# Kernel optimization log

Hardware: AMD Instinct MI355X
Metric: run time of the kernel (lower is better)

Reference implementation:

```python
import jax, jax.numpy as jnp
import numpy as np

DIM, FFN, GC, NSET, K = 48, 2, 2, 32, 3
HID = DIM * FFN          # 96 hidden features
G = HID // GC            # 48 groups in KBA
CG = HID // G            # 2 channels per group
INTERC = 24              # min(dim, 24)
B, H, W = 4, 128, 128


def _conv(x, w, b=None, groups=1, pad=0):
    out = jax.lax.conv_general_dilated(
        x, w, (1, 1), [(pad, pad), (pad, pad)],
        dimension_numbers=('NCHW', 'OIHW', 'NCHW'),
        feature_group_count=groups)
    if b is not None:
        out = out + b[None, :, None, None]
    return out


def _kba(x, att, k, g, bb, ww):
    # x: [B,c,H,W], att: [B,nset,H,W], bb: [1,nset,c], ww: [1,nset,c*c//g*k*k]
    Bz, c, Hh, Ww = x.shape
    KK = k * k
    cg = c // g
    P = Hh * Ww
    a = att.reshape(Bz, -1, P).transpose(0, 2, 1)                     # [B,P,nset]
    bias = jnp.einsum('bpn,nc->bpc', a, bb[0])                        # [B,P,c]
    attk = jnp.einsum('bpn,nm->bpm', a, ww[0]).reshape(Bz, P, g, cg, cg * KK)
    pd = k // 2
    xp = jnp.pad(x, ((0, 0), (0, 0), (pd, pd), (pd, pd)))
    # im2col patches, torch.unfold layout: channel-major, kernel row-major
    patches = jnp.stack([xp[:, :, i:i + Hh, j:j + Ww]
                         for i in range(k) for j in range(k)], axis=2)  # [B,c,KK,H,W]
    uf = patches.reshape(Bz, g, cg * KK, P).transpose(0, 3, 1, 2)       # [B,P,g,cg*KK]
    out = jnp.einsum('bpgom,bpgm->bpgo', attk, uf).reshape(Bz, P, c) + bias
    return out.transpose(0, 2, 1).reshape(Bz, c, Hh, Ww)


def setup_inputs() -> dict:
    key = jax.random.key(0)
    ks = jax.random.split(key, 20)
    s = 0.05
    inp = {
        'x': jax.random.normal(ks[0], (B, DIM, H, W), jnp.float32),
        'dw1_w': jax.random.normal(ks[1], (HID, DIM, 1, 1), jnp.float32) * s,
        'dw2_w': jax.random.normal(ks[2], (HID, 1, 3, 3), jnp.float32) * s,
        'proj_w': jax.random.normal(ks[3], (DIM, HID, 1, 1), jnp.float32) * s,
        'sca_w': jax.random.normal(ks[4], (HID, HID, 1, 1), jnp.float32) * s,
        'sca_b': jax.random.normal(ks[5], (HID,), jnp.float32) * s,
        'c1_w1': jax.random.normal(ks[6], (HID, DIM, 1, 1), jnp.float32) * s,
        'c1_w2': jax.random.normal(ks[7], (HID, 1, 3, 3), jnp.float32) * s,
        'kba_w': jax.random.normal(ks[8], (1, NSET, HID * CG * K * K), jnp.float32) * s,
        'kba_b': jax.random.normal(ks[9], (1, NSET, HID), jnp.float32) * s,
        'c2_w1': jax.random.normal(ks[10], (INTERC, DIM // INTERC, 3, 3), jnp.float32) * s,
        'c2_b1': jax.random.normal(ks[11], (INTERC,), jnp.float32) * s,
        'c2_w2': jax.random.normal(ks[12], (NSET, INTERC // 2, 1, 1), jnp.float32) * s,
        'c2_b2': jax.random.normal(ks[13], (NSET,), jnp.float32) * s,
        'c211_w': jax.random.normal(ks[14], (NSET, DIM, 1, 1), jnp.float32) * s,
        'c211_b': jax.random.normal(ks[15], (NSET,), jnp.float32) * s,
        'attgamma': jnp.full((1, NSET, 1, 1), 0.01, jnp.float32),
        'ga1': jnp.full((1, HID, 1, 1), 0.01, jnp.float32),
    }
    return inp


def reference(x, dw1_w, dw2_w, proj_w, sca_w, sca_b, c1_w1, c1_w2,
              kba_w, kba_b, c2_w1, c2_b1, c2_w2, c2_b2,
              c211_w, c211_b, attgamma, ga1):
    # dwconv branch: 1x1 -> depthwise 3x3
    x1 = _conv(_conv(x, dw1_w), dw2_w, groups=HID, pad=1)
    # attention map branch: grouped 3x3 -> SimpleGate -> 1x1, scaled + skip 1x1
    t = _conv(x, c2_w1, c2_b1, groups=INTERC, pad=1)
    t1, t2 = jnp.split(t, 2, axis=1)
    t = _conv(t1 * t2, c2_w2, c2_b2)
    att = t * attgamma + _conv(x, c211_w, c211_b)
    # conv1 branch feeding KBA
    uf = _conv(_conv(x, c1_w1), c1_w2, groups=HID, pad=1)
    x2 = _kba(uf, att, K, G, kba_b, kba_w) * ga1 + uf
    comb = jax.nn.gelu(x1, approximate=False) * x2
    pooled = jnp.mean(comb, axis=(2, 3), keepdims=True)
    comb = comb * _conv(pooled, sca_w, sca_b)
    return _conv(comb, proj_w)
```

## Files before the change

kernel.cpp:

```cpp
#include <hip/hip_runtime.h>
#include <math.h>

#define BB 4
#define HH 128
#define WW 128
#define HWP (HH*WW)
#define DIMC 48
#define HIDC 96
#define NSETC 32

#define XS_W 27
#define HS_W 102
#define US_W 102

typedef __attribute__((ext_vector_type(8))) short bf16x8;
typedef __attribute__((ext_vector_type(4))) float f32x4;
typedef __attribute__((ext_vector_type(2))) float f32x2;

static __device__ __forceinline__ unsigned short f2bf(float f) {
    union { float f; unsigned u; } v; v.f = f;
    unsigned r = (v.u + 0x7FFFu + ((v.u >> 16) & 1u)) >> 16;
    return (unsigned short)r;
}
static __device__ __forceinline__ unsigned rnd_bf(float f) {
    union { float f; unsigned u; } v; v.f = f;
    return v.u + 0x8000u;
}
static __device__ __forceinline__ unsigned pack2bf(float lo, float hi) {
    return __builtin_amdgcn_perm(rnd_bf(hi), rnd_bf(lo), 0x07060302u);
}
static __device__ __forceinline__ void st_bf_hi(unsigned short* p, float f) {
    *p = (unsigned short)(rnd_bf(f) >> 16);
}
static __device__ __forceinline__ float bf2f(unsigned short u) {
    union { unsigned u; float f; } v; v.u = ((unsigned)u) << 16;
    return v.f;
}
static __device__ __forceinline__ float bfpair_lo(unsigned pr) {
    union { unsigned u; float f; } v; v.u = pr << 16; return v.f;
}
static __device__ __forceinline__ float bfpair_hi(unsigned pr) {
    union { unsigned u; float f; } v; v.u = pr & 0xffff0000u; return v.f;
}
static __device__ __forceinline__ float gelu(float x) {
    return 0.5f * x * (1.0f + erff(x * 0.70710678118654752f));
}

__global__ __launch_bounds__(256) void k_prep(
    const float* __restrict__ x,
    const float* __restrict__ kbaw, const float* __restrict__ kbab,
    const float* __restrict__ dw1w, const float* __restrict__ c1w1,
    const float* __restrict__ ga1,  const float* __restrict__ c211w,
    const float* __restrict__ c2w2, const float* __restrict__ c2b2,
    const float* __restrict__ c211b, const float* __restrict__ attg,
    unsigned short* __restrict__ Bpk, unsigned short* __restrict__ Bpw,
    unsigned short* __restrict__ Aps, unsigned short* __restrict__ Ag,
    unsigned* __restrict__ x_p, float* __restrict__ pooled)
{
    __shared__ unsigned ts[256 * 26];
    int blk = blockIdx.x, tid = threadIdx.x;
    if (blk < 300) {
        int t = blk * 256 + tid;
        if (t < 61440) {
            int j = t & 7, lane = (t >> 3) & 63, tile = t >> 9;
            int chunk = tile / 10, nt = tile - chunk * 10;
            int m = lane & 15, qn = lane >> 4;
            int lc = 4 * nt + (m & 3);
            int o = lc / 20, tt = lc % 20;
            int c = (m >> 2) * 24 + 2 * chunk + o;
            int n = qn * 8 + j;
            float v = 0.f;
            if (tt < 18)       v = kbaw[n * 1728 + (c >> 1) * 36 + (c & 1) * 18 + tt] * ga1[c];
            else if (tt == 18) v = kbab[n * 96 + c] * ga1[c];
            Bpk[t] = f2bf(v);
        } else if (t < 73728) {
            int u = t - 61440;
            int s = u / 6144;
            int rem = u % 6144;
            int nt = rem >> 9;
            int lane = (rem >> 3) & 63, j = rem & 7;
            int k = s * 32 + ((lane >> 4) << 3) + j;
            int col = (nt << 4) + (lane & 15);
            float v = 0.f;
            if (k < 48) v = (col < 96) ? dw1w[col * 48 + k] : c1w1[(col - 96) * 48 + k];
            Bpw[u] = f2bf(v);
        } else if (t < 75776) {
            int u = t - 73728;
            int j = u & 7, lane = (u >> 3) & 63, tile = u >> 9;
            int kt = tile >> 1, nt2 = tile & 1;
            int m = lane & 15, qn = lane >> 4;
            int n = 8 * (m >> 2) + 4 * nt2 + (m & 3);
            int k = kt * 32 + qn * 8 + j;
            Aps[u] = f2bf(k < 48 ? c211w[n * 48 + k] : 0.f);
        } else if (t < 76800) {
            int u = t - 75776;
            int j = u & 7, lane = (u >> 3) & 63, nt2 = u >> 9;
            int m = lane & 15, qn = lane >> 4;
            int n = 8 * (m >> 2) + 4 * nt2 + (m & 3);
            int k = qn * 8 + j;
            float v = 0.f;
            if (k < 12)       v = c2w2[n * 12 + k] * attg[n];
            else if (k == 12) v = c2b2[n] * attg[n] + c211b[n];
            Ag[u] = f2bf(v);
        }
    } else {
        int xblk = blk - 300;
        if (xblk == 0) {
            for (int i = tid; i < BB * HIDC; i += 256) pooled[i] = 0.f;
        }
        int b = xblk >> 6;
        int p0 = (xblk & 63) << 8;
        const float* xb = x + (size_t)b * DIMC * HWP + p0;
        #pragma unroll
        for (int c2 = 0; c2 < 24; ++c2) {
            float lo = xb[(2 * c2) * HWP + tid];
            float hi = xb[(2 * c2 + 1) * HWP + tid];
            ts[tid * 26 + c2] = pack2bf(lo, hi);
        }
        __syncthreads();
        unsigned* dst = x_p + ((size_t)b * HWP + p0) * 24;
        for (int idx = tid; idx < 256 * 24; idx += 256) {
            int px = idx / 24, j2 = idx - px * 24;
            dst[px * 24 + j2] = ts[px * 26 + j2];
        }
    }
}

__global__ __launch_bounds__(512, 2) void k_mff(
    const unsigned* __restrict__ x_p,
    const uint4* __restrict__ BpkA, const uint4* __restrict__ Bpw,
    const uint4* __restrict__ Aps,  const uint4* __restrict__ Ag,
    const float* __restrict__ c1w2, const float* __restrict__ dw2w,
    const float* __restrict__ c2w1, const float* __restrict__ c2b1,
    unsigned* __restrict__ comb_bf, float* __restrict__ pooled)
{
    __shared__ __attribute__((aligned(16))) unsigned xs[144 * XS_W];
    __shared__ __attribute__((aligned(16))) unsigned short hsw[144 * HS_W];
    __shared__ unsigned short us2p[100 * US_W];
    __shared__ float wls[864 + 432 + 24];
    __shared__ float pooled_s[96];

    int lane = threadIdx.x, wy = threadIdx.y;
    int tid = wy * 64 + lane;
    int blk = blockIdx.x;
    int b = blk >> 8, ty = (blk >> 4) & 15, tx = blk & 15;
    int q = lane >> 4, i16 = lane & 15;
    int wh = wy >> 2;
    int wp = wy & 3;

    float* wats  = wls + 864;
    float* c2b1s = wls + 864 + 432;
    float* att_tf = (float*)hsw;

    if (tid < 96) pooled_s[tid] = 0.f;
    for (int idx = tid; idx < 864; idx += 512) {
        int t5 = idx / 96, c = idx - t5 * 96;
        wls[idx] = dw2w[c * 9 + t5];
    }
    for (int idx = tid; idx < 216; idx += 512) {
        int g = idx / 9, tap = idx - g * 9;
        wats[idx * 2]     = c2w1[g * 18 + tap];
        wats[idx * 2 + 1] = c2w1[g * 18 + 9 + tap];
    }
    if (tid < 24) c2b1s[tid] = c2b1[tid];
    for (int idx = tid; idx < 144 * 12; idx += 512) {
        int pos = idx / 12, jp = idx - pos * 12;
        int gy = ty * 8 - 2 + pos / 12, gx = tx * 8 - 2 + pos % 12;
        uint2 v = {0u, 0u};
        if (((unsigned)gy < (unsigned)HH) & ((unsigned)gx < (unsigned)WW))
            v = *(const uint2*)&x_p[((size_t)b * HWP + gy * WW + gx) * 24 + jp * 2];
        xs[pos * XS_W + jp * 2]     = v.x;
        xs[pos * XS_W + jp * 2 + 1] = v.y;
    }
    __syncthreads();

    int p_t = wp * 16 + i16;
    int pyT = p_t >> 3, pxT = p_t & 7;
    int gp = (ty * 8 + pyT) * WW + tx * 8 + pxT;
    uint4 z4 = {0u, 0u, 0u, 0u};

    #pragma unroll
    for (int ci = 0; ci < 3; ++ci) {
        int g = q * 6 + wh * 3 + ci;
        float acc = c2b1s[g];
        #pragma unroll
        for (int di = 0; di < 3; ++di)
          #pragma unroll
          for (int dj = 0; dj < 3; ++dj) {
              unsigned pr = xs[((pyT + 1 + di) * 12 + pxT + 1 + dj) * XS_W + g];
              f32x2 w2 = *(const f32x2*)&wats[(g * 9 + di * 3 + dj) * 2];
              acc += w2.x * bfpair_lo(pr) + w2.y * bfpair_hi(pr);
          }
        att_tf[p_t * XS_W + g] = acc;
    }
    __syncthreads();

    bf16x8 afrag;
    {
        int p26 = p_t * XS_W;
        unsigned tgd[4];
        #pragma unroll
        for (int i2 = 0; i2 < 4; ++i2) {
            int k0 = q * 8 + 2 * i2;
            int k1 = k0 + 1;
            float v0 = (k0 < 12) ? att_tf[p26 + k0] * att_tf[p26 + 12 + k0] : (k0 == 12 ? 1.f : 0.f);
            float v1 = (k1 < 12) ? att_tf[p26 + k1] * att_tf[p26 + 12 + k1] : (k1 == 12 ? 1.f : 0.f);
            tgd[i2] = pack2bf(v0, v1);
        }
        uint4 tgr = {tgd[0], tgd[1], tgd[2], tgd[3]};
        bf16x8 btg = __builtin_bit_cast(bf16x8, tgr);

        int cen = (pyT + 2) * 12 + (pxT + 2);
        int cb = cen * XS_W + q * 4;
        uint4 bx0r = {xs[cb], xs[cb + 1], xs[cb + 2], xs[cb + 3]};
        uint4 bx1r = z4;
        if (q < 2) {
            int cb2 = cen * XS_W + 16 + q * 4;
            bx1r.x = xs[cb2]; bx1r.y = xs[cb2 + 1]; bx1r.z = xs[cb2 + 2]; bx1r.w = xs[cb2 + 3];
        }
        bf16x8 bx0 = __builtin_bit_cast(bf16x8, bx0r);
        bf16x8 bx1 = __builtin_bit_cast(bf16x8, bx1r);

        float attv[8];
        #pragma unroll
        for (int nt2 = 0; nt2 < 2; ++nt2) {
            bf16x8 ag  = __builtin_bit_cast(bf16x8, Ag[nt2 * 64 + lane]);
            bf16x8 as0 = __builtin_bit_cast(bf16x8, Aps[nt2 * 64 + lane]);
            bf16x8 as1 = __builtin_bit_cast(bf16x8, Aps[(2 + nt2) * 64 + lane]);
            f32x4 z = {0.f, 0.f, 0.f, 0.f};
            f32x4 c = __builtin_amdgcn_mfma_f32_16x16x32_bf16(ag, btg, z, 0, 0, 0);
            c = __builtin_amdgcn_mfma_f32_16x16x32_bf16(as1, bx1, c, 0, 0, 0);
            c = __builtin_amdgcn_mfma_f32_16x16x32_bf16(as0, bx0, c, 0, 0, 0);
            #pragma unroll
            for (int r = 0; r < 4; ++r) attv[nt2 * 4 + r] = c[r];
        }
        uint4 au = {pack2bf(attv[0], attv[1]), pack2bf(attv[2], attv[3]),
                    pack2bf(attv[4], attv[5]), pack2bf(attv[6], attv[7])};
        afrag = __builtin_bit_cast(bf16x8, au);
    }
    __syncthreads();

    {
        int nA = (wy == 0) ? 2 : 1;
        #pragma unroll 1
        for (int rr = 0; rr < nA; ++rr) {
            int rg = rr ? 8 : wy;
            int hp = rg * 16 + i16;
            int ab = hp * XS_W + q * 4;
            uint4 a0r = {xs[ab], xs[ab + 1], xs[ab + 2], xs[ab + 3]};
            uint4 a1r = z4;
            if (q < 2) {
                int ab2 = hp * XS_W + 16 + q * 4;
                a1r.x = xs[ab2]; a1r.y = xs[ab2 + 1]; a1r.z = xs[ab2 + 2]; a1r.w = xs[ab2 + 3];
            }
            bf16x8 a0 = __builtin_bit_cast(bf16x8, a0r);
            bf16x8 a1 = __builtin_bit_cast(bf16x8, a1r);
            int rowb = rg * 16 + 4 * q;
            #pragma unroll
            for (int nt = 0; nt < 6; ++nt) {
                bf16x8 b0 = __builtin_bit_cast(bf16x8, Bpw[(size_t)((6 + nt) << 6) + lane]);
                bf16x8 b1 = __builtin_bit_cast(bf16x8, Bpw[(size_t)((18 + nt) << 6) + lane]);
                f32x4 z = {0.f, 0.f, 0.f, 0.f};
                f32x4 c = __builtin_amdgcn_mfma_f32_16x16x32_bf16(a1, b1, z, 0, 0, 0);
                c = __builtin_amdgcn_mfma_f32_16x16x32_bf16(a0, b0, c, 0, 0, 0);
                #pragma unroll
                for (int r = 0; r < 4; ++r)
                    st_bf_hi(&hsw[(rowb + r) * HS_W + nt * 16 + i16], c[r]);
            }
        }
    }
    __syncthreads();

    #pragma unroll 1
    for (int it = 0; it < 3; ++it) {
        int su = wy * 3 + it;
        int cq = su >> 1;
        const float* w9 = c1w2 + cq * 8 * 9;
        int hp2 = (su & 1) * 50 + lane;
        if (lane < 50) {
            int py2 = hp2 / 10, px2 = hp2 - py2 * 10;
            float acc[8];
            #pragma unroll
            for (int c = 0; c < 8; ++c) acc[c] = 0.f;
            #pragma unroll
            for (int di = 0; di < 3; ++di)
              #pragma unroll
              for (int dj = 0; dj < 3; ++dj) {
                  int rb = ((py2 + di) * 12 + px2 + dj) * HS_W + cq * 8;
                  unsigned pp[4];
                  pp[0] = *(const unsigned*)&hsw[rb];
                  pp[1] = *(const unsigned*)&hsw[rb + 2];
                  pp[2] = *(const unsigned*)&hsw[rb + 4];
                  pp[3] = *(const unsigned*)&hsw[rb + 6];
                  #pragma unroll
                  for (int c2 = 0; c2 < 4; ++c2) {
                      acc[2*c2]   += w9[(2*c2) * 9 + di * 3 + dj]   * bfpair_lo(pp[c2]);
                      acc[2*c2+1] += w9[(2*c2+1) * 9 + di * 3 + dj] * bfpair_hi(pp[c2]);
                  }
              }
            int wb = hp2 * US_W + cq * 8;
            *(unsigned*)&us2p[wb]     = pack2bf(acc[0], acc[1]);
            *(unsigned*)&us2p[wb + 2] = pack2bf(acc[2], acc[3]);
            *(unsigned*)&us2p[wb + 4] = pack2bf(acc[4], acc[5]);
            *(unsigned*)&us2p[wb + 6] = pack2bf(acc[6], acc[7]);
        }
    }
    __syncthreads();

    if (wy < 7) {
        int rg = wy;
        int hp = rg * 16 + i16;
        bool okp = hp < 100;
        int hy = hp / 10, hx = hp - hy * 10;
        int pos = okp ? ((hy + 1) * 12 + hx + 1) : 0;
        int ab = pos * XS_W + q * 4;
        uint4 a0r = {xs[ab], xs[ab + 1], xs[ab + 2], xs[ab + 3]};
        uint4 a1r = z4;
        if (q < 2) {
            int ab2 = pos * XS_W + 16 + q * 4;
            a1r.x = xs[ab2]; a1r.y = xs[ab2 + 1]; a1r.z = xs[ab2 + 2]; a1r.w = xs[ab2 + 3];
        }
        bf16x8 a0 = __builtin_bit_cast(bf16x8, a0r);
        bf16x8 a1 = __builtin_bit_cast(bf16x8, a1r);
        int rowb = rg * 16 + 4 * q;
        #pragma unroll
        for (int nt = 0; nt < 6; ++nt) {
            bf16x8 b0 = __builtin_bit_cast(bf16x8, Bpw[(size_t)(nt << 6) + lane]);
            bf16x8 b1 = __builtin_bit_cast(bf16x8, Bpw[(size_t)((12 + nt) << 6) + lane]);
            f32x4 z = {0.f, 0.f, 0.f, 0.f};
            f32x4 c = __builtin_amdgcn_mfma_f32_16x16x32_bf16(a1, b1, z, 0, 0, 0);
            c = __builtin_amdgcn_mfma_f32_16x16x32_bf16(a0, b0, c, 0, 0, 0);
            #pragma unroll
            for (int r = 0; r < 4; ++r)
                st_bf_hi(&hsw[(rowb + r) * HS_W + nt * 16 + i16], c[r]);
        }
    }
    __syncthreads();

    f32x2 greg[6];
    {
        int base = q * 24 + wh * 12;
        #pragma unroll
        for (int cc = 0; cc < 6; ++cc) {
            int c0 = base + 2 * cc;
            f32x2 acc = {0.f, 0.f};
            #pragma unroll
            for (int di = 0; di < 3; ++di)
              #pragma unroll
              for (int dj = 0; dj < 3; ++dj) {
                  unsigned pr = *(const unsigned*)&hsw[((pyT + di) * 10 + pxT + dj) * HS_W + c0];
                  f32x2 hv = {bfpair_lo(pr), bfpair_hi(pr)};
                  f32x2 wv = *(const f32x2*)&wls[(di * 3 + dj) * 96 + c0];
                  acc += wv * hv;
              }
            greg[cc].x = gelu(acc.x);
            greg[cc].y = gelu(acc.y);
        }
    }

    unsigned* cmb = comb_bf + ((size_t)b * HWP + gp) * 48 + q * 12;
    int hpC = (pyT + 1) * 10 + pxT + 1;

    #pragma unroll
    for (int cl = 0; cl < 6; ++cl) {
        int chunk = wh * 6 + cl;
        int c0 = q * 24 + 2 * chunk;
        float u[18];
        #pragma unroll
        for (int i = 0; i < 3; ++i)
          #pragma unroll
          for (int j = 0; j < 3; ++j) {
              unsigned pr = *(const unsigned*)&us2p[((pyT + i) * 10 + pxT + j) * US_W + c0];
              u[i * 3 + j]     = bfpair_lo(pr);
              u[9 + i * 3 + j] = bfpair_hi(pr);
          }
        unsigned sp = *(const unsigned*)&us2p[hpC * US_W + c0];
        f32x4 cf[10];
        #pragma unroll
        for (int nt = 0; nt < 10; ++nt) {
            bf16x8 aW = __builtin_bit_cast(bf16x8, BpkA[(size_t)((chunk * 10 + nt) << 6) + lane]);
            f32x4 z = {0.f, 0.f, 0.f, 0.f};
            cf[nt] = __builtin_amdgcn_mfma_f32_16x16x32_bf16(aW, afrag, z, 0, 0, 0);
        }
        float acc0 = cf[4][2];
        float acc1 = cf[9][2];
        #pragma unroll
        for (int m = 0; m < 16; ++m) {
            acc0 += cf[m >> 2][m & 3]       * u[m];
            acc1 += cf[5 + (m >> 2)][m & 3] * u[m];
        }
        acc0 += cf[4][0] * u[16] + cf[4][1] * u[17];
        acc1 += cf[9][0] * u[16] + cf[9][1] * u[17];

        float x20 = acc0 + bfpair_lo(sp);
        float x21 = acc1 + bfpair_hi(sp);
        float cv0 = greg[cl].x * x20;
        float cv1 = greg[cl].y * x21;
        cmb[chunk] = pack2bf(cv0, cv1);
        float r0 = cv0, r1 = cv1;
        #pragma unroll
        for (int s = 1; s < 16; s <<= 1) {
            r0 += __shfl_xor(r0, s, 64);
            r1 += __shfl_xor(r1, s, 64);
        }
        if (i16 == 0) {
            atomicAdd(&pooled_s[c0], r0);
            atomicAdd(&pooled_s[c0 + 1], r1);
        }
    }
    __syncthreads();
    if (tid < 96) atomicAdd(&pooled[b * HIDC + tid], pooled_s[tid]);
}

__global__ __launch_bounds__(256) void k_final(
    const unsigned* __restrict__ comb_bf, const float* __restrict__ pooled,
    const float* __restrict__ scaw, const float* __restrict__ scab,
    const float* __restrict__ projw, float* __restrict__ out)
{
    __shared__ float svs[96];
    __shared__ float cs[96][66];
    int tid = threadIdx.x;
    int blk = blockIdx.x;
    int p0 = blk * 64;
    int b = p0 >> 14;
    if (tid < 96) {
        float dot = 0.f;
        const float* pr = pooled + b * 96;
        const float* wr = scaw + tid * 96;
        #pragma unroll 4
        for (int k = 0; k < 96; ++k) dot += wr[k] * pr[k];
        svs[tid] = scab[tid] + dot * (1.0f / (float)HWP);
    }
    __syncthreads();
    for (int idx = tid; idx < 64 * 12; idx += 256) {
        int px = idx / 12, cq = idx - px * 12;
        uint4 v = *(const uint4*)&comb_bf[(size_t)(p0 + px) * 48 + cq * 4];
        int k0 = cq * 8;
        unsigned pp[4] = {v.x, v.y, v.z, v.w};
        #pragma unroll
        for (int j = 0; j < 4; ++j) {
            cs[k0 + 2*j][px]     = bfpair_lo(pp[j]) * svs[k0 + 2*j];
            cs[k0 + 2*j + 1][px] = bfpair_hi(pp[j]) * svs[k0 + 2*j + 1];
        }
    }
    __syncthreads();
    int l = tid & 63, w = tid >> 6;
    int o0 = w * 12;
    float acc[12];
    #pragma unroll
    for (int o = 0; o < 12; ++o) acc[o] = 0.f;
    #pragma unroll 4
    for (int k = 0; k < 96; ++k) {
        float v = cs[k][l];
        #pragma unroll
        for (int o = 0; o < 12; ++o)
            acc[o] += projw[(o0 + o) * 96 + k] * v;
    }
    float* ob = out + (size_t)b * DIMC * HWP + (p0 & 16383) + l;
    #pragma unroll
    for (int o = 0; o < 12; ++o)
        ob[(o0 + o) * HWP] = acc[o];
}

extern "C" void kernel_launch(void* const* d_in, const int* in_sizes, int n_in,
                              void* d_out, int out_size, void* d_ws, size_t ws_size,
                              hipStream_t stream)
{
    const float* x     = (const float*)d_in[0];
    const float* dw1w  = (const float*)d_in[1];
    const float* dw2w  = (const float*)d_in[2];
    const float* projw = (const float*)d_in[3];
    const float* scaw  = (const float*)d_in[4];
    const float* scab  = (const float*)d_in[5];
    const float* c1w1  = (const float*)d_in[6];
    const float* c1w2  = (const float*)d_in[7];
    const float* kbaw  = (const float*)d_in[8];
    const float* kbab  = (const float*)d_in[9];
    const float* c2w1  = (const float*)d_in[10];
    const float* c2b1  = (const float*)d_in[11];
    const float* c2w2  = (const float*)d_in[12];
    const float* c2b2  = (const float*)d_in[13];
    const float* c211w = (const float*)d_in[14];
    const float* c211b = (const float*)d_in[15];
    const float* attg  = (const float*)d_in[16];
    const float* ga1   = (const float*)d_in[17];

    unsigned* x_p     = (unsigned*)d_ws;
    unsigned* comb_bf = x_p + (size_t)BB * HWP * 24;
    float* pooled     = (float*)(comb_bf + (size_t)BB * HWP * 48);
    unsigned short* BpkA = (unsigned short*)(pooled + BB * HIDC);
    unsigned short* Bpw  = BpkA + 61440;
    unsigned short* Aps  = Bpw + 12288;
    unsigned short* Ag   = Aps + 2048;

    k_prep <<<556,  256, 0, stream>>>(x, kbaw, kbab, dw1w, c1w1, ga1, c211w, c2w2, c2b2,
                                      c211b, attg, BpkA, Bpw, Aps, Ag, x_p, pooled);
    k_mff  <<<1024, dim3(64,8,1), 0, stream>>>(x_p, (const uint4*)BpkA, (const uint4*)Bpw,
                                               (const uint4*)Aps, (const uint4*)Ag,
                                               c1w2, dw2w, c2w1, c2b1, comb_bf, pooled);
    k_final<<<1024, 256, 0, stream>>>(comb_bf, pooled, scaw, scab, projw, (float*)d_out);
}
```

Before: 200.8 us.

## Raise occupancy bound, spread tail MFMA tile across waves, prefetch KBA weights

Raises the launch-bounds minimum blocks per CU from 2 to 4, which caps registers per thread so more blocks can be resident. The leftover ninth row tile of the 1x1 conv, previously done entirely by wave 0, is split across waves 1-6 with one n-tile each to balance load. The KBA weight fragments are double-buffered in registers, loaded one chunk ahead, to hide global load latency behind the MFMAs. The tighter register cap combined with the new 80-register prefetch buffer risks spilling, and LDS use may still limit how many blocks actually fit.

Measured after the change: 212.9 us. 1.06x slower.

```diff
diff --git a/kernel.cpp b/kernel.cpp
--- a/kernel.cpp
+++ b/kernel.cpp
@@ -126,7 +126,7 @@
     }
 }
 
-__global__ __launch_bounds__(512, 2) void k_mff(
+__global__ __launch_bounds__(512, 4) void k_mff(
     const unsigned* __restrict__ x_p,
     const uint4* __restrict__ BpkA, const uint4* __restrict__ Bpw,
     const uint4* __restrict__ Aps,  const uint4* __restrict__ Ag,
@@ -241,10 +241,8 @@
     __syncthreads();
 
     {
-        int nA = (wy == 0) ? 2 : 1;
-        #pragma unroll 1
-        for (int rr = 0; rr < nA; ++rr) {
-            int rg = rr ? 8 : wy;
+        {
+            int rg = wy;
             int hp = rg * 16 + i16;
             int ab = hp * XS_W + q * 4;
             uint4 a0r = {xs[ab], xs[ab + 1], xs[ab + 2], xs[ab + 3]};
@@ -267,6 +265,28 @@
                 for (int r = 0; r < 4; ++r)
                     st_bf_hi(&hsw[(rowb + r) * HS_W + nt * 16 + i16], c[r]);
             }
+        }
+        if (wy >= 1 && wy <= 6) {
+            int hp = 128 + i16;
+            int ab = hp * XS_W + q * 4;
+            uint4 a0r = {xs[ab], xs[ab + 1], xs[ab + 2], xs[ab + 3]};
+            uint4 a1r = z4;
+            if (q < 2) {
+                int ab2 = hp * XS_W + 16 + q * 4;
+                a1r.x = xs[ab2]; a1r.y = xs[ab2 + 1]; a1r.z = xs[ab2 + 2]; a1r.w = xs[ab2 + 3];
+            }
+            bf16x8 a0 = __builtin_bit_cast(bf16x8, a0r);
+            bf16x8 a1 = __builtin_bit_cast(bf16x8, a1r);
+            int rowb = 128 + 4 * q;
+            int nt = wy - 1;
+            bf16x8 b0 = __builtin_bit_cast(bf16x8, Bpw[(size_t)((6 + nt) << 6) + lane]);
+            bf16x8 b1 = __builtin_bit_cast(bf16x8, Bpw[(size_t)((18 + nt) << 6) + lane]);
+            f32x4 z = {0.f, 0.f, 0.f, 0.f};
+            f32x4 c = __builtin_amdgcn_mfma_f32_16x16x32_bf16(a1, b1, z, 0, 0, 0);
+            c = __builtin_amdgcn_mfma_f32_16x16x32_bf16(a0, b0, c, 0, 0, 0);
+            #pragma unroll
+            for (int r = 0; r < 4; ++r)
+                st_bf_hi(&hsw[(rowb + r) * HS_W + nt * 16 + i16], c[r]);
         }
     }
     __syncthreads();
@@ -360,10 +380,20 @@
 
     unsigned* cmb = comb_bf + ((size_t)b * HWP + gp) * 48 + q * 12;
     int hpC = (pyT + 1) * 10 + pxT + 1;
+    const uint4* bpk_base = BpkA + (size_t)(wh * 60) * 64 + lane;
+
+    uint4 buf[2][10];
+    #pragma unroll
+    for (int nt = 0; nt < 10; ++nt) buf[0][nt] = bpk_base[(size_t)nt << 6];
 
     #pragma unroll
     for (int cl = 0; cl < 6; ++cl) {
         int chunk = wh * 6 + cl;
+        if (cl < 5) {
+            #pragma unroll
+            for (int nt = 0; nt < 10; ++nt)
+                buf[(cl + 1) & 1][nt] = bpk_base[(size_t)(((cl + 1) * 10 + nt)) << 6];
+        }
         int c0 = q * 24 + 2 * chunk;
         float u[18];
         #pragma unroll
@@ -378,7 +408,7 @@
         f32x4 cf[10];
         #pragma unroll
         for (int nt = 0; nt < 10; ++nt) {
-            bf16x8 aW = __builtin_bit_cast(bf16x8, BpkA[(size_t)((chunk * 10 + nt) << 6) + lane]);
+            bf16x8 aW = __builtin_bit_cast(bf16x8, buf[cl & 1][nt]);
             f32x4 z = {0.f, 0.f, 0.f, 0.f};
             cf[nt] = __builtin_amdgcn_mfma_f32_16x16x32_bf16(aW, afrag, z, 0, 0, 0);
         }
```
